# Optimization experiments

Hardware: AMD Instinct MI355X
Metric: run time of the kernel (lower is better)

## Reference

```python
import jax, jax.numpy as jnp
import numpy as np

N = 100000   # nodes
E = 1600000  # edges
F = 128      # input features
H = 128      # hidden
O = 64       # output classes
BN_EPS = 1e-5


def gcn_conv(x, edge_index, W, b, n_nodes):
    """PyG-style GCNConv: h = D^-1/2 (A+I) D^-1/2 (x W) + b."""
    h = x @ W  # [N, out]
    row = jnp.concatenate([edge_index[0], jnp.arange(n_nodes)])  # add self loops
    col = jnp.concatenate([edge_index[1], jnp.arange(n_nodes)])
    deg = jax.ops.segment_sum(jnp.ones_like(row, dtype=h.dtype), row, num_segments=n_nodes)
    dinv = jnp.where(deg > 0, jax.lax.rsqrt(deg), 0.0)
    norm = dinv[row] * dinv[col]                 # [E+N]
    msg = h[col] * norm[:, None]                 # gather + scale
    out = jax.ops.segment_sum(msg, row, num_segments=n_nodes)  # scatter-add
    return out + b


def batch_norm(x, gamma, beta):
    mean = jnp.mean(x, axis=0)
    var = jnp.var(x, axis=0)
    return (x - mean) * jax.lax.rsqrt(var + BN_EPS) * gamma + beta


def setup_inputs() -> dict:
    key = jax.random.key(0)
    ks = jax.random.split(key, 10)
    x = jax.random.normal(ks[0], (N, F), dtype=jnp.float32)
    edge_index = jax.random.randint(ks[1], (2, E), 0, N, dtype=jnp.int64)
    W1 = jax.random.normal(ks[2], (F, H), dtype=jnp.float32) / np.sqrt(F)
    b1 = jnp.zeros((H,), dtype=jnp.float32)
    gamma1 = jnp.ones((H,), dtype=jnp.float32)
    beta1 = jnp.zeros((H,), dtype=jnp.float32)
    W2 = jax.random.normal(ks[3], (H, H), dtype=jnp.float32) / np.sqrt(H)
    b2 = jnp.zeros((H,), dtype=jnp.float32)
    W3 = jax.random.normal(ks[4], (H, O), dtype=jnp.float32) / np.sqrt(H)
    b3 = jnp.zeros((O,), dtype=jnp.float32)
    return {"x": x, "edge_index": edge_index, "W1": W1, "b1": b1,
            "gamma1": gamma1, "beta1": beta1, "W2": W2, "b2": b2,
            "W3": W3, "b3": b3}


def reference(x, edge_index, W1, b1, gamma1, beta1, W2, b2, W3, b3):
    h = gcn_conv(x, edge_index, W1, b1, N)
    h = jax.nn.relu(batch_norm(h, gamma1, beta1))
    h = gcn_conv(h, edge_index, W2, b2, N)
    h = jax.nn.relu(h)
    out = h @ W3 + b3  # final Linear classifier head [N, O]
    return out
```

## Files before the change

kernel.cpp:

```cpp
#include <hip/hip_runtime.h>

#define NN 100000
#define EE 1600000
#define HN 128
#define OO 64
#define SB 256
#define NBUCK 196
#define CH 4096
#define SLAB 16384

typedef __attribute__((ext_vector_type(8))) short bf16x8;
typedef __attribute__((ext_vector_type(4))) float f32x4;

__device__ __forceinline__ unsigned short f2bf(float f){
  unsigned u = __float_as_uint(f);
  return (unsigned short)((u + 0x7FFFu + ((u >> 16) & 1u)) >> 16);
}
__device__ __forceinline__ float bflo(unsigned u){ return __uint_as_float(u << 16); }
__device__ __forceinline__ float bfhi(unsigned u){ return __uint_as_float(u & 0xFFFF0000u); }

#define CB ((EE + CH - 1)/CH)
#define GB ((NN + 127)/128)

__global__ __launch_bounds__(256) void k_fused(const int* __restrict__ rows, const int* __restrict__ cols,
                                               int* __restrict__ pcur, unsigned* __restrict__ ebuf,
                                               const float* __restrict__ x, const float* __restrict__ W1,
                                               const float* __restrict__ W2, const float* __restrict__ W3,
                                               unsigned short* __restrict__ Wp2, unsigned short* __restrict__ Wp3,
                                               unsigned* __restrict__ hbf){
  __shared__ char lds[65536];
  const int t = threadIdx.x;

  if (blockIdx.x < CB){
    int* bc    = (int*)lds;
    int* boff  = (int*)(lds + 1024);
    int* ccur  = (int*)(lds + 2048);
    int* gbase = (int*)(lds + 3072);
    uint2* stage = (uint2*)(lds + 4096);
    const int base = blockIdx.x * CH;
    const int nval = min(CH, EE - base);

    for (int i = t; i < NBUCK; i += 256) bc[i] = 0;
    __syncthreads();

    int er[16], ec[16];
    #pragma unroll
    for (int j = 0; j < 16; ++j){
      int i = j*256 + t;
      if (i < nval){
        er[j] = rows[base+i]; ec[j] = cols[base+i];
        atomicAdd(&bc[er[j] >> 9], 1);
      } else er[j] = -1;
    }
    __syncthreads();

    if (t < 64){
      int lane = t, run = 0;
      for (int c = 0; c < NBUCK; c += 64){
        int i = c + lane;
        int v = (i < NBUCK) ? bc[i] : 0;
        int s = v;
        #pragma unroll
        for (int d = 1; d < 64; d <<= 1){ int u = __shfl_up(s, d); if (lane >= d) s += u; }
        if (i < NBUCK) boff[i] = run + s - v;
        run += __shfl(s, 63);
      }
    }
    __syncthreads();
    if (t < NBUCK){
      gbase[t] = bc[t] ? (t*SLAB + atomicAdd(&pcur[t], bc[t])) : 0;
      ccur[t]  = boff[t];
    }
    __syncthreads();
    #pragma unroll
    for (int j = 0; j < 16; ++j){
      if (er[j] >= 0){
        int b = er[j] >> 9;
        int p = atomicAdd(&ccur[b], 1);
        stage[p] = make_uint2((unsigned)er[j], (unsigned)ec[j]);
      }
    }
    __syncthreads();
    for (int i = t; i < nval; i += 256){
      uint2 e = stage[i];
      int b = (int)(e.x >> 9);
      unsigned pk = ((e.x & 511u) << 17) | e.y;
      ebuf[gbase[b] + (i - boff[b])] = pk;
    }

    int b = blockIdx.x;
    if (b < 12){
      const float* W = (b < 8) ? W2 : W3;
      unsigned short* Wp = (b < 8) ? Wp2 : Wp3;
      int outc = (b < 8) ? 128 : 64;
      int i0 = (b < 8) ? b*256 : (b-8)*256;
      int i = i0 + t;
      if (i < 16*outc){
        int kb = i / outc, n = i - kb*outc;
        unsigned pk[4];
        #pragma unroll
        for (int jj = 0; jj < 4; ++jj){
          unsigned lo = f2bf(W[(size_t)(kb*8 + 2*jj)*outc + n]);
          unsigned hi = f2bf(W[(size_t)(kb*8 + 2*jj+1)*outc + n]);
          pk[jj] = lo | (hi << 16);
        }
        *reinterpret_cast<uint4*>(Wp + (size_t)i*8) = make_uint4(pk[0],pk[1],pk[2],pk[3]);
      }
    }
  } else {
    char* AsB = lds;
    char* WsB = lds + 32768;
    const int row0 = (int)(blockIdx.x - CB) * 128;

    {
      #pragma unroll
      for (int it = 0; it < 8; ++it){
        int i = it*256 + t;
        int kb = i >> 7, n = i & 127;
        unsigned pk[4];
        #pragma unroll
        for (int j = 0; j < 4; ++j){
          unsigned lo = f2bf(W1[(size_t)(kb*8 + 2*j)*128 + n]);
          unsigned hi = f2bf(W1[(size_t)(kb*8 + 2*j+1)*128 + n]);
          pk[j] = lo | (hi << 16);
        }
        *reinterpret_cast<uint4*>(WsB + (size_t)i*16) = make_uint4(pk[0],pk[1],pk[2],pk[3]);
      }
    }
    {
      #pragma unroll
      for (int g = 0; g < 16; ++g){
        int f = g*256 + t;
        int r = f >> 5;
        int c4 = f & 31;
        int row = row0 + r;
        int rc = row < NN ? row : NN-1;
        float4 v = *reinterpret_cast<const float4*>(x + (size_t)rc*HN + c4*4);
        unsigned p0 = (unsigned)f2bf(v.x) | ((unsigned)f2bf(v.y) << 16);
        unsigned p1 = (unsigned)f2bf(v.z) | ((unsigned)f2bf(v.w) << 16);
        int boffb = (c4*8) ^ ((r & 7) << 4);
        *reinterpret_cast<uint2*>(AsB + r*256 + boffb) = make_uint2(p0, p1);
      }
    }
    __syncthreads();

    const int wv = t >> 6;
    const int l  = t & 63;
    const int lm = l & 15;
    const int lk = l >> 4;

    f32x4 acc[2][8];
    #pragma unroll
    for (int mi=0;mi<2;++mi)
      #pragma unroll
      for (int ni=0;ni<8;++ni) acc[mi][ni] = (f32x4){0.f,0.f,0.f,0.f};

    #pragma unroll
    for (int ks = 0; ks < 4; ++ks){
      bf16x8 af[2];
      #pragma unroll
      for (int mi=0;mi<2;++mi){
        int R = wv*32 + mi*16 + lm;
        int boffb = (ks*64 + lk*16) ^ ((R & 7) << 4);
        af[mi] = *reinterpret_cast<const bf16x8*>(AsB + R*256 + boffb);
      }
      int kb = ks*4 + lk;
      #pragma unroll
      for (int ni=0;ni<8;++ni){
        int n = ni*16 + lm;
        bf16x8 bfr = *reinterpret_cast<const bf16x8*>(WsB + (size_t)(kb*128 + n)*16);
        acc[0][ni] = __builtin_amdgcn_mfma_f32_16x16x32_bf16(af[0], bfr, acc[0][ni], 0,0,0);
        acc[1][ni] = __builtin_amdgcn_mfma_f32_16x16x32_bf16(af[1], bfr, acc[1][ni], 0,0,0);
      }
    }

    #pragma unroll
    for (int mi=0;mi<2;++mi){
      #pragma unroll
      for (int j=0;j<4;++j){
        int grow = row0 + wv*32 + mi*16 + lk*4 + j;
        if (grow >= NN) continue;
        unsigned short* po = (unsigned short*)hbf + (size_t)grow*HN;
        #pragma unroll
        for (int ni=0;ni<8;++ni)
          po[ni*16 + lm] = f2bf(acc[mi][ni][j]);
      }
    }
  }
}

__global__ __launch_bounds__(256) void k_build(const unsigned* __restrict__ ebuf,
                                               const int* __restrict__ pcur,
                                               int* __restrict__ row_start, int* __restrict__ cnt,
                                               float* __restrict__ dinv, int* __restrict__ csr_col){
  __shared__ int hist[512];
  __shared__ int cur[512];
  __shared__ int sCbase;
  const int b = blockIdx.x;
  const int row0 = b << 9;
  const int nrow = min(512, NN - row0);
  const int ebase = b * SLAB;
  const int ne = pcur[b];
  const int t = threadIdx.x;

  if (t < 64){
    int acc = 0;
    for (int i = t; i < b; i += 64) acc += pcur[i];
    #pragma unroll
    for (int d = 32; d; d >>= 1) acc += __shfl_xor(acc, d);
    if (t == 0) sCbase = acc;
  }
  for (int i = t; i < nrow; i += 256) hist[i] = 0;
  __syncthreads();
  for (int i = t; i < ne; i += 256)
    atomicAdd(&hist[ebuf[ebase+i] >> 17], 1);
  __syncthreads();

  if (t < 64){
    int lane = t, run = 0;
    for (int c = 0; c < nrow; c += 64){
      int i = c + lane;
      int v = (i < nrow) ? hist[i] : 0;
      int s = v;
      #pragma unroll
      for (int d = 1; d < 64; d <<= 1){ int u = __shfl_up(s, d); if (lane >= d) s += u; }
      if (i < nrow) cur[i] = run + s - v;
      run += __shfl(s, 63);
    }
  }
  __syncthreads();
  const int cbase = sCbase;
  for (int i = t; i < nrow; i += 256){
    int h = hist[i];
    int r = row0 + i;
    cnt[r] = h;
    dinv[r] = rsqrtf((float)(h+1));
    row_start[r] = cbase + cur[i];
    cur[i] += cbase;
  }
  __syncthreads();
  for (int i = t; i < ne; i += 256){
    unsigned e = ebuf[ebase+i];
    int p = atomicAdd(&cur[e >> 17], 1);
    csr_col[p] = (int)(e & 0x1FFFFu);
  }
}

__global__ __launch_bounds__(256) void k_aggd(const unsigned* __restrict__ h,
                                              const int* __restrict__ row_start,
                                              const int* __restrict__ cnt,
                                              const int* __restrict__ col,
                                              const float* __restrict__ dinv,
                                              const float* __restrict__ bias,
                                              unsigned* __restrict__ outv){
  int wib  = __builtin_amdgcn_readfirstlane((int)(threadIdx.x >> 6));
  int wid  = blockIdx.x*4 + wib;
  int lane = threadIdx.x & 63;
  if (wid >= NN) return;
  int s = row_start[wid];
  int e = s + cnt[wid];
  float dr = dinv[wid];
  const unsigned* hp = h + lane;
  float ax, ay;
  {
    unsigned u = hp[(size_t)wid*64];
    ax = dr*bflo(u); ay = dr*bfhi(u);
  }
  int p = s;
  for (; p+7 < e; p += 8){
    unsigned uu[8]; float dd[8];
    #pragma unroll
    for (int j=0;j<8;++j){ int c = col[p+j]; dd[j] = dinv[c]; uu[j] = hp[(size_t)c*64]; }
    #pragma unroll
    for (int j=0;j<8;++j){ ax = fmaf(bflo(uu[j]), dd[j], ax); ay = fmaf(bfhi(uu[j]), dd[j], ay); }
  }
  for (; p+3 < e; p += 4){
    unsigned uu[4]; float dd[4];
    #pragma unroll
    for (int j=0;j<4;++j){ int c = col[p+j]; dd[j] = dinv[c]; uu[j] = hp[(size_t)c*64]; }
    #pragma unroll
    for (int j=0;j<4;++j){ ax = fmaf(bflo(uu[j]), dd[j], ax); ay = fmaf(bfhi(uu[j]), dd[j], ay); }
  }
  for (; p < e; ++p){
    int c = col[p]; float d = dinv[c];
    unsigned u = hp[(size_t)c*64];
    ax = fmaf(bflo(u), d, ax); ay = fmaf(bfhi(u), d, ay);
  }
  float2 bb = *reinterpret_cast<const float2*>(bias + 2*lane);
  float ox = ax*dr + bb.x, oy = ay*dr + bb.y;
  outv[(size_t)wid*64 + lane] = (unsigned)f2bf(ox) | ((unsigned)f2bf(oy) << 16);
}

__global__ __launch_bounds__(256) void k_aggmm(const unsigned* __restrict__ h,
                                               const int* __restrict__ row_start,
                                               const int* __restrict__ cnt,
                                               const int* __restrict__ col,
                                               const float* __restrict__ dinv,
                                               const float* __restrict__ b2,
                                               const unsigned short* __restrict__ Wp3,
                                               const float* __restrict__ b3,
                                               float* __restrict__ out){
  __shared__ char AsB[32*256];
  const int t = threadIdx.x;
  const int wv = __builtin_amdgcn_readfirstlane(t >> 6);
  const int lane = t & 63;
  const int tile = blockIdx.x * 32;

  for (int k = 0; k < 8; ++k){
    int wid = tile + wv*8 + k;
    int s = row_start[wid];
    int e = s + cnt[wid];
    float dr = dinv[wid];
    const unsigned* hp = h + lane;
    float ax, ay;
    { unsigned u = hp[(size_t)wid*64]; ax = bflo(u); ay = bfhi(u); }
    int p = s;
    for (; p+7 < e; p += 8){
      unsigned uu[8];
      #pragma unroll
      for (int j=0;j<8;++j) uu[j] = hp[(size_t)col[p+j]*64];
      #pragma unroll
      for (int j=0;j<8;++j){ ax += bflo(uu[j]); ay += bfhi(uu[j]); }
    }
    for (; p+3 < e; p += 4){
      unsigned uu[4];
      #pragma unroll
      for (int j=0;j<4;++j) uu[j] = hp[(size_t)col[p+j]*64];
      #pragma unroll
      for (int j=0;j<4;++j){ ax += bflo(uu[j]); ay += bfhi(uu[j]); }
    }
    for (; p < e; ++p){
      unsigned u = hp[(size_t)col[p]*64];
      ax += bflo(u); ay += bfhi(u);
    }
    float2 bb = *reinterpret_cast<const float2*>(b2 + 2*lane);
    float ox = fmaxf(ax*dr + bb.x, 0.f);
    float oy = fmaxf(ay*dr + bb.y, 0.f);
    int r = wv*8 + k;
    unsigned pk = (unsigned)f2bf(ox) | ((unsigned)f2bf(oy) << 16);
    *reinterpret_cast<unsigned*>(AsB + r*256 + ((lane*4) ^ ((r & 7) << 4))) = pk;
  }
  __syncthreads();

  const int lm = lane & 15;
  const int lk = lane >> 4;
  const int mb  = wv >> 1;
  const int nb2 = (wv & 1) * 2;
  f32x4 acc[2] = {(f32x4){0.f,0.f,0.f,0.f},(f32x4){0.f,0.f,0.f,0.f}};
  const bf16x8* WpV = reinterpret_cast<const bf16x8*>(Wp3);

  #pragma unroll
  for (int ks = 0; ks < 4; ++ks){
    int R = mb*16 + lm;
    bf16x8 af = *reinterpret_cast<const bf16x8*>(AsB + R*256 + ((ks*64 + lk*16) ^ ((R & 7) << 4)));
    int kb = ks*4 + lk;
    #pragma unroll
    for (int ni = 0; ni < 2; ++ni){
      int n = (nb2+ni)*16 + lm;
      bf16x8 bfr = WpV[kb*OO + n];
      acc[ni] = __builtin_amdgcn_mfma_f32_16x16x32_bf16(af, bfr, acc[ni], 0,0,0);
    }
  }

  #pragma unroll
  for (int ni = 0; ni < 2; ++ni){
    int gcol = (nb2+ni)*16 + lm;
    float bb = b3[gcol];
    #pragma unroll
    for (int j = 0; j < 4; ++j){
      int grow = tile + mb*16 + lk*4 + j;
      out[(size_t)grow*OO + gcol] = acc[ni][j] + bb;
    }
  }
}

__global__ __launch_bounds__(256) void k_mgemm2(const unsigned* __restrict__ Av,
                                                const unsigned short* __restrict__ Wp,
                                                const float* __restrict__ scale,
                                                const float* __restrict__ shiftv,
                                                const float* __restrict__ dinv,
                                                unsigned* __restrict__ Cv){
  __shared__ char AsB[32768];
  const int t = threadIdx.x;
  const int row0 = blockIdx.x * 128;

  {
    const uint4* A = (const uint4*)Av;
    const int c8 = t & 15;
    const int k0 = c8*8;
    float sc[8], sh[8];
    #pragma unroll
    for (int j=0;j<8;++j){ sc[j]=scale[k0+j]; sh[j]=shiftv[k0+j]; }
    #pragma unroll
    for (int g = 0; g < 8; ++g){
      int f = g*256 + t;
      int r = f >> 4;
      int row = row0 + r;
      int rc = row < NN ? row : NN-1;
      uint4 q = A[(size_t)rc*16 + c8];
      float vf[8] = { bflo(q.x),bfhi(q.x),bflo(q.y),bfhi(q.y),
                      bflo(q.z),bfhi(q.z),bflo(q.w),bfhi(q.w) };
      #pragma unroll
      for (int j=0;j<8;++j) vf[j] = fmaxf(fmaf(vf[j], sc[j], sh[j]), 0.f);
      unsigned pk[4];
      #pragma unroll
      for (int j=0;j<4;++j)
        pk[j] = (unsigned)f2bf(vf[2*j]) | ((unsigned)f2bf(vf[2*j+1]) << 16);
      int boffb = (c8*16) ^ ((r & 7) << 4);
      *reinterpret_cast<uint4*>(AsB + r*256 + boffb) = make_uint4(pk[0],pk[1],pk[2],pk[3]);
    }
  }
  __syncthreads();

  const int wv = t >> 6;
  const int l  = t & 63;
  const int lm = l & 15;
  const int lk = l >> 4;

  f32x4 acc[2][8];
  #pragma unroll
  for (int mi=0;mi<2;++mi)
    #pragma unroll
    for (int ni=0;ni<8;++ni) acc[mi][ni] = (f32x4){0.f,0.f,0.f,0.f};

  const bf16x8* WpV = reinterpret_cast<const bf16x8*>(Wp);

  #pragma unroll
  for (int ks = 0; ks < 4; ++ks){
    bf16x8 af[2];
    #pragma unroll
    for (int mi=0;mi<2;++mi){
      int R = wv*32 + mi*16 + lm;
      int boffb = (ks*64 + lk*16) ^ ((R & 7) << 4);
      af[mi] = *reinterpret_cast<const bf16x8*>(AsB + R*256 + boffb);
    }
    int kb = ks*4 + lk;
    #pragma unroll
    for (int ni=0;ni<8;++ni){
      int n = ni*16 + lm;
      bf16x8 bfr = WpV[kb*128 + n];
      acc[0][ni] = __builtin_amdgcn_mfma_f32_16x16x32_bf16(af[0], bfr, acc[0][ni], 0,0,0);
      acc[1][ni] = __builtin_amdgcn_mfma_f32_16x16x32_bf16(af[1], bfr, acc[1][ni], 0,0,0);
    }
  }

  #pragma unroll
  for (int mi=0;mi<2;++mi){
    #pragma unroll
    for (int j=0;j<4;++j){
      int grow = row0 + wv*32 + mi*16 + lk*4 + j;
      if (grow >= NN) continue;
      float dr = dinv[grow];
      unsigned short* po = (unsigned short*)Cv + (size_t)grow*HN;
      #pragma unroll
      for (int ni=0;ni<8;++ni)
        po[ni*16 + lm] = f2bf(acc[mi][ni][j] * dr);
    }
  }
}

__global__ __launch_bounds__(256) void k_stats(const unsigned* __restrict__ a,
                                               float* __restrict__ ps, float* __restrict__ pq){
  __shared__ float l0[256], l1[256], m0[256], m1[256];
  int c = threadIdx.x & 63;
  int grp = threadIdx.x >> 6;
  float s0=0.f,s1=0.f,q0=0.f,q1=0.f;
  for (int r = blockIdx.x*4 + grp; r < NN; r += SB*4){
    unsigned u = a[(size_t)r*64 + c];
    float v0 = bflo(u), v1 = bfhi(u);
    s0 += v0; s1 += v1; q0 = fmaf(v0,v0,q0); q1 = fmaf(v1,v1,q1);
  }
  l0[threadIdx.x]=s0; l1[threadIdx.x]=s1; m0[threadIdx.x]=q0; m1[threadIdx.x]=q1;
  __syncthreads();
  if (grp==0){
    #pragma unroll
    for (int g=1;g<4;++g){ s0+=l0[g*64+c]; s1+=l1[g*64+c]; q0+=m0[g*64+c]; q1+=m1[g*64+c]; }
    ps[blockIdx.x*128 + 2*c]   = s0; ps[blockIdx.x*128 + 2*c+1] = s1;
    pq[blockIdx.x*128 + 2*c]   = q0; pq[blockIdx.x*128 + 2*c+1] = q1;
  }
}

__global__ __launch_bounds__(128) void k_bnfinal(const float* __restrict__ ps, const float* __restrict__ pq,
                                                 const float* __restrict__ gamma, const float* __restrict__ beta,
                                                 float* __restrict__ scale, float* __restrict__ shiftv){
  int c = threadIdx.x;
  float s=0.f, q=0.f;
  for (int b=0;b<SB;b++){ s += ps[b*128+c]; q += pq[b*128+c]; }
  float mean = s * (1.0f/NN);
  float var  = q * (1.0f/NN) - mean*mean;
  float inv  = rsqrtf(var + 1e-5f);
  float sc = gamma[c]*inv;
  scale[c]  = sc;
  shiftv[c] = beta[c] - mean*sc;
}

extern "C" void kernel_launch(void* const* d_in, const int* in_sizes, int n_in,
                              void* d_out, int out_size, void* d_ws, size_t ws_size,
                              hipStream_t stream) {
  const float* x      = (const float*)d_in[0];
  const int*   ei     = (const int*)d_in[1];
  const int*   rows   = ei;
  const int*   cols   = ei + EE;
  const float* W1     = (const float*)d_in[2];
  const float* b1     = (const float*)d_in[3];
  const float* gamma1 = (const float*)d_in[4];
  const float* beta1  = (const float*)d_in[5];
  const float* W2     = (const float*)d_in[6];
  const float* b2     = (const float*)d_in[7];
  const float* W3     = (const float*)d_in[8];
  const float* b3     = (const float*)d_in[9];
  float* out = (float*)d_out;

  char* w = (char*)d_ws;
  float* buf0      = (float*)w; w += (size_t)NN*HN*4;
  float* buf1      = (float*)w; w += (size_t)NN*HN*4;
  int*   csr_col   = (int*)w;   w += (size_t)EE*4;
  int*   row_start = (int*)w;   w += (size_t)NN*4;
  int*   cnt       = (int*)w;   w += (size_t)NN*4;
  float* dinv      = (float*)w; w += (size_t)NN*4;
  float* ps        = (float*)w; w += (size_t)SB*128*4;
  float* pq        = (float*)w; w += (size_t)SB*128*4;
  float* scale     = (float*)w; w += 1024;
  float* shiftv    = (float*)w; w += 1024;
  int*   scr0      = (int*)w;   w += 4096;
  unsigned short* Wp2 = (unsigned short*)w; w += 128*128*2;
  unsigned short* Wp3 = (unsigned short*)w; w += 128*64*2;
  int* pcur = scr0;
  unsigned* hbf  = (unsigned*)buf0;
  unsigned* ebuf = (unsigned*)buf0 + (size_t)NN*64;
  unsigned* abf  = (unsigned*)buf1;

  (void)hipMemsetAsync(scr0, 0, 4096, stream);

  const int AB = NN/4, FB = NN/32;

  k_fused<<<CB + GB, 256, 0, stream>>>(rows, cols, pcur, ebuf, x, W1, W2, W3, Wp2, Wp3, hbf);
  k_build<<<NBUCK, 256, 0, stream>>>(ebuf, pcur, row_start, cnt, dinv, csr_col);

  k_aggd<<<AB, 256, 0, stream>>>(hbf, row_start, cnt, csr_col, dinv, b1, abf);
  k_stats<<<SB, 256, 0, stream>>>(abf, ps, pq);
  k_bnfinal<<<1, 128, 0, stream>>>(ps, pq, gamma1, beta1, scale, shiftv);

  k_mgemm2<<<GB, 256, 0, stream>>>(abf, Wp2, scale, shiftv, dinv, hbf);

  k_aggmm<<<FB, 256, 0, stream>>>(hbf, row_start, cnt, csr_col, dinv, b2, Wp3, b3, out);
}
```

Baseline: 240.0 us.

## Fuse BN stats and finalize via last-block atomics; shrink aggmm tiles to 16 rows

Merges the batch-norm partial-sum kernel and the single-block finalize kernel into one kernel. Blocks atomically accumulate channel sums, and the last block to finish (found with an atomic counter) computes scale and shift, which removes one launch and the serial pass over 256 partials. The aggregate+matmul kernel now processes 16 rows per block with each wave owning one 16-column output slice, doubling the grid for more parallelism in the gather phase. Float atomics make the summation order nondeterministic, and the smaller tiles mean more W3 fragment loads per row.

```diff
diff --git a/kernel.cpp b/kernel.cpp
--- a/kernel.cpp
+++ b/kernel.cpp
@@ -291,6 +291,47 @@
   outv[(size_t)wid*64 + lane] = (unsigned)f2bf(ox) | ((unsigned)f2bf(oy) << 16);
 }
 
+__global__ __launch_bounds__(256) void k_statsfin(const unsigned* __restrict__ a,
+                                                  float* __restrict__ gps, float* __restrict__ gpq,
+                                                  int* __restrict__ done,
+                                                  const float* __restrict__ gamma, const float* __restrict__ beta,
+                                                  float* __restrict__ scale, float* __restrict__ shiftv){
+  __shared__ float l0[256], l1[256], m0[256], m1[256];
+  __shared__ int lastFlag;
+  int c = threadIdx.x & 63;
+  int grp = threadIdx.x >> 6;
+  float s0=0.f,s1=0.f,q0=0.f,q1=0.f;
+  for (int r = blockIdx.x*4 + grp; r < NN; r += SB*4){
+    unsigned u = a[(size_t)r*64 + c];
+    float v0 = bflo(u), v1 = bfhi(u);
+    s0 += v0; s1 += v1; q0 = fmaf(v0,v0,q0); q1 = fmaf(v1,v1,q1);
+  }
+  l0[threadIdx.x]=s0; l1[threadIdx.x]=s1; m0[threadIdx.x]=q0; m1[threadIdx.x]=q1;
+  __syncthreads();
+  if (grp==0){
+    #pragma unroll
+    for (int g=1;g<4;++g){ s0+=l0[g*64+c]; s1+=l1[g*64+c]; q0+=m0[g*64+c]; q1+=m1[g*64+c]; }
+    atomicAdd(&gps[2*c],   s0);
+    atomicAdd(&gps[2*c+1], s1);
+    atomicAdd(&gpq[2*c],   q0);
+    atomicAdd(&gpq[2*c+1], q1);
+  }
+  __threadfence();
+  if (threadIdx.x == 0) lastFlag = (atomicAdd(done, 1) == SB-1);
+  __syncthreads();
+  if (lastFlag && threadIdx.x < 128){
+    int ch = threadIdx.x;
+    float s = atomicAdd(&gps[ch], 0.0f);
+    float q = atomicAdd(&gpq[ch], 0.0f);
+    float mean = s * (1.0f/NN);
+    float var  = q * (1.0f/NN) - mean*mean;
+    float inv  = rsqrtf(var + 1e-5f);
+    float sc = gamma[ch]*inv;
+    scale[ch]  = sc;
+    shiftv[ch] = beta[ch] - mean*sc;
+  }
+}
+
 __global__ __launch_bounds__(256) void k_aggmm(const unsigned* __restrict__ h,
                                                const int* __restrict__ row_start,
                                                const int* __restrict__ cnt,
@@ -300,14 +341,14 @@
                                                const unsigned short* __restrict__ Wp3,
                                                const float* __restrict__ b3,
                                                float* __restrict__ out){
-  __shared__ char AsB[32*256];
+  __shared__ char AsB[16*256];
   const int t = threadIdx.x;
   const int wv = __builtin_amdgcn_readfirstlane(t >> 6);
   const int lane = t & 63;
-  const int tile = blockIdx.x * 32;
-
-  for (int k = 0; k < 8; ++k){
-    int wid = tile + wv*8 + k;
+  const int tile = blockIdx.x * 16;
+
+  for (int k = 0; k < 4; ++k){
+    int wid = tile + wv*4 + k;
     int s = row_start[wid];
     int e = s + cnt[wid];
     float dr = dinv[wid];
@@ -336,7 +377,7 @@
     float2 bb = *reinterpret_cast<const float2*>(b2 + 2*lane);
     float ox = fmaxf(ax*dr + bb.x, 0.f);
     float oy = fmaxf(ay*dr + bb.y, 0.f);
-    int r = wv*8 + k;
+    int r = wv*4 + k;
     unsigned pk = (unsigned)f2bf(ox) | ((unsigned)f2bf(oy) << 16);
     *reinterpret_cast<unsigned*>(AsB + r*256 + ((lane*4) ^ ((r & 7) << 4))) = pk;
   }
@@ -344,33 +385,24 @@
 
   const int lm = lane & 15;
   const int lk = lane >> 4;
-  const int mb  = wv >> 1;
-  const int nb2 = (wv & 1) * 2;
-  f32x4 acc[2] = {(f32x4){0.f,0.f,0.f,0.f},(f32x4){0.f,0.f,0.f,0.f}};
+  f32x4 acc = (f32x4){0.f,0.f,0.f,0.f};
   const bf16x8* WpV = reinterpret_cast<const bf16x8*>(Wp3);
 
   #pragma unroll
   for (int ks = 0; ks < 4; ++ks){
-    int R = mb*16 + lm;
+    int R = lm;
     bf16x8 af = *reinterpret_cast<const bf16x8*>(AsB + R*256 + ((ks*64 + lk*16) ^ ((R & 7) << 4)));
     int kb = ks*4 + lk;
-    #pragma unroll
-    for (int ni = 0; ni < 2; ++ni){
-      int n = (nb2+ni)*16 + lm;
-      bf16x8 bfr = WpV[kb*OO + n];
-      acc[ni] = __builtin_amdgcn_mfma_f32_16x16x32_bf16(af, bfr, acc[ni], 0,0,0);
-    }
-  }
-
+    bf16x8 bfr = WpV[kb*OO + wv*16 + lm];
+    acc = __builtin_amdgcn_mfma_f32_16x16x32_bf16(af, bfr, acc, 0,0,0);
+  }
+
+  int gcol = wv*16 + lm;
+  float bb = b3[gcol];
   #pragma unroll
-  for (int ni = 0; ni < 2; ++ni){
-    int gcol = (nb2+ni)*16 + lm;
-    float bb = b3[gcol];
-    #pragma unroll
-    for (int j = 0; j < 4; ++j){
-      int grow = tile + mb*16 + lk*4 + j;
-      out[(size_t)grow*OO + gcol] = acc[ni][j] + bb;
-    }
+  for (int j = 0; j < 4; ++j){
+    int grow = tile + lk*4 + j;
+    out[(size_t)grow*OO + gcol] = acc[j] + bb;
   }
 }
 
@@ -457,41 +489,6 @@
         po[ni*16 + lm] = f2bf(acc[mi][ni][j] * dr);
     }
   }
-}
-
-__global__ __launch_bounds__(256) void k_stats(const unsigned* __restrict__ a,
-                                               float* __restrict__ ps, float* __restrict__ pq){
-  __shared__ float l0[256], l1[256], m0[256], m1[256];
-  int c = threadIdx.x & 63;
-  int grp = threadIdx.x >> 6;
-  float s0=0.f,s1=0.f,q0=0.f,q1=0.f;
-  for (int r = blockIdx.x*4 + grp; r < NN; r += SB*4){
-    unsigned u = a[(size_t)r*64 + c];
-    float v0 = bflo(u), v1 = bfhi(u);
-    s0 += v0; s1 += v1; q0 = fmaf(v0,v0,q0); q1 = fmaf(v1,v1,q1);
-  }
-  l0[threadIdx.x]=s0; l1[threadIdx.x]=s1; m0[threadIdx.x]=q0; m1[threadIdx.x]=q1;
-  __syncthreads();
-  if (grp==0){
-    #pragma unroll
-    for (int g=1;g<4;++g){ s0+=l0[g*64+c]; s1+=l1[g*64+c]; q0+=m0[g*64+c]; q1+=m1[g*64+c]; }
-    ps[blockIdx.x*128 + 2*c]   = s0; ps[blockIdx.x*128 + 2*c+1] = s1;
-    pq[blockIdx.x*128 + 2*c]   = q0; pq[blockIdx.x*128 + 2*c+1] = q1;
-  }
-}
-
-__global__ __launch_bounds__(128) void k_bnfinal(const float* __restrict__ ps, const float* __restrict__ pq,
-                                                 const float* __restrict__ gamma, const float* __restrict__ beta,
-                                                 float* __restrict__ scale, float* __restrict__ shiftv){
-  int c = threadIdx.x;
-  float s=0.f, q=0.f;
-  for (int b=0;b<SB;b++){ s += ps[b*128+c]; q += pq[b*128+c]; }
-  float mean = s * (1.0f/NN);
-  float var  = q * (1.0f/NN) - mean*mean;
-  float inv  = rsqrtf(var + 1e-5f);
-  float sc = gamma[c]*inv;
-  scale[c]  = sc;
-  shiftv[c] = beta[c] - mean*sc;
 }
 
 extern "C" void kernel_launch(void* const* d_in, const int* in_sizes, int n_in,
@@ -518,28 +515,28 @@
   int*   row_start = (int*)w;   w += (size_t)NN*4;
   int*   cnt       = (int*)w;   w += (size_t)NN*4;
   float* dinv      = (float*)w; w += (size_t)NN*4;
-  float* ps        = (float*)w; w += (size_t)SB*128*4;
-  float* pq        = (float*)w; w += (size_t)SB*128*4;
   float* scale     = (float*)w; w += 1024;
   float* shiftv    = (float*)w; w += 1024;
   int*   scr0      = (int*)w;   w += 4096;
   unsigned short* Wp2 = (unsigned short*)w; w += 128*128*2;
   unsigned short* Wp3 = (unsigned short*)w; w += 128*64*2;
-  int* pcur = scr0;
+  int*   pcur = scr0;
+  int*   done = scr0 + 256;
+  float* gps  = (float*)(scr0 + 320);
+  float* gpq  = (float*)(scr0 + 448);
   unsigned* hbf  = (unsigned*)buf0;
   unsigned* ebuf = (unsigned*)buf0 + (size_t)NN*64;
   unsigned* abf  = (unsigned*)buf1;
 
   (void)hipMemsetAsync(scr0, 0, 4096, stream);
 
-  const int AB = NN/4, FB = NN/32;
+  const int AB = NN/4, FB = NN/16;
 
   k_fused<<<CB + GB, 256, 0, stream>>>(rows, cols, pcur, ebuf, x, W1, W2, W3, Wp2, Wp3, hbf);
   k_build<<<NBUCK, 256, 0, stream>>>(ebuf, pcur, row_start, cnt, dinv, csr_col);
 
   k_aggd<<<AB, 256, 0, stream>>>(hbf, row_start, cnt, csr_col, dinv, b1, abf);
-  k_stats<<<SB, 256, 0, stream>>>(abf, ps, pq);
-  k_bnfinal<<<1, 128, 0, stream>>>(ps, pq, gamma1, beta1, scale, shiftv);
+  k_statsfin<<<SB, 256, 0, stream>>>(abf, gps, gpq, done, gamma1, beta1, scale, shiftv);
 
   k_mgemm2<<<GB, 256, 0, stream>>>(abf, Wp2, scale, shiftv, dinv, hbf);
 
```

Result: slower. 248.4 us (+3.5%).
